# Optimization experiments

Measured on AMD Instinct MI355X. Metric: run time of the kernel, lower is better.

The kernel has to match this reference:

```python
import jax, jax.numpy as jnp
import numpy as np

B, L, H, E, V = 32, 1024, 1024, 512, 8192

def setup_inputs() -> dict:
    key = jax.random.key(0)
    k1, k2, k3, k4 = jax.random.split(key, 4)
    x = jax.random.randint(k1, (B, L), 0, V)
    hidden = jnp.zeros((B, H), dtype=jnp.float32)  # equivalent to hidden=None path
    embedding = jax.random.normal(k2, (V, E), dtype=jnp.float32)
    W_h = jax.random.normal(k3, (E + H, H), dtype=jnp.float32) * 0.01
    b_h = jnp.zeros((H,), dtype=jnp.float32)
    W_o = jax.random.normal(k4, (H, V), dtype=jnp.float32) * 0.01
    b_o = jnp.zeros((V,), dtype=jnp.float32)
    return {"x": x, "hidden": hidden, "embedding": embedding,
            "W_h": W_h, "b_h": b_h, "W_o": W_o, "b_o": b_o}

def reference(x, hidden, embedding, W_h, b_h, W_o, b_o):
    # x: [B, L] int; hidden: [B, H]
    x_embed = embedding[x]                       # [B, L, E]
    x_tl = jnp.swapaxes(x_embed, 0, 1)           # [L, B, E] time-major

    def step(h, x_t):
        # concat + matmul + bias + tanh, one timestep
        combined = jnp.concatenate([x_t, h], axis=1)   # [B, E+H]
        h_new = jnp.tanh(combined @ W_h + b_h)         # [B, H]
        return h_new, h_new

    final_hidden, outs = jax.lax.scan(step, hidden, x_tl)  # outs: [L, B, H]
    output = jnp.swapaxes(outs, 0, 1)                       # [B, L, H]
    logits = output @ W_o + b_o                             # [B, L, V]
    return logits, final_hidden
```

## Files before the change

kernel.cpp:

```cpp
#include <hip/hip_runtime.h>
#include <hip/hip_bf16.h>

typedef unsigned short u16;
typedef unsigned int   u32;
typedef unsigned long long u64;
typedef __attribute__((ext_vector_type(8))) __bf16 bf16x8;
typedef __attribute__((ext_vector_type(4))) float   f32x4;

#define GLOAD16(gp, lp) __builtin_amdgcn_global_load_lds( \
    (__attribute__((address_space(1))) void*)(gp),        \
    (__attribute__((address_space(3))) void*)(lp), 16, 0, 0)

static __device__ __forceinline__ u16 f2bf(float f) {
  __bf16 b = (__bf16)f;
  return __builtin_bit_cast(u16, b);
}
static __device__ __forceinline__ f32x4 mfma16(bf16x8 a, bf16x8 b, f32x4 c) {
  return __builtin_amdgcn_mfma_f32_16x16x32_bf16(a, b, c, 0, 0, 0);
}


__global__ __launch_bounds__(256) void k_cvt_emb(const float* __restrict__ s,
                                                 u16* __restrict__ d) {
  int i = (blockIdx.x * 256 + threadIdx.x) * 4;
  float4 v = *(const float4*)(s + i);
  d[i] = f2bf(v.x); d[i+1] = f2bf(v.y); d[i+2] = f2bf(v.z); d[i+3] = f2bf(v.w);
}

__global__ __launch_bounds__(256) void k_tr_wh(const float* __restrict__ Wh,
                                               u16* __restrict__ WhxT,
                                               u16* __restrict__ WhhT) {
  __shared__ float tile[32][33];
  int bx = blockIdx.x & 31;
  int be = blockIdx.x >> 5;
  int tx = threadIdx.x & 31, ty = threadIdx.x >> 5;
  #pragma unroll
  for (int s = 0; s < 32; s += 8)
    tile[ty + s][tx] = Wh[(size_t)(be*32 + ty + s) * 1024 + bx*32 + tx];
  __syncthreads();
  #pragma unroll
  for (int s = 0; s < 32; s += 8) {
    int e = be*32 + tx;
    int j = bx*32 + ty + s;
    u16 v = f2bf(tile[tx][ty + s]);
    if (e < 512) WhxT[(size_t)j * 512 + e] = v;
    else         WhhT[(size_t)j * 1024 + (e - 512)] = v;
  }
}

__global__ __launch_bounds__(256) void k_tr_wo(const float* __restrict__ Wo,
                                               u16* __restrict__ WoT) {
  __shared__ float tile[32][33];
  int bx = blockIdx.x & 255;
  int by = blockIdx.x >> 8;
  int tx = threadIdx.x & 31, ty = threadIdx.x >> 5;
  #pragma unroll
  for (int s = 0; s < 32; s += 8)
    tile[ty + s][tx] = Wo[(size_t)(by*32 + ty + s) * 8192 + bx*32 + tx];
  __syncthreads();
  #pragma unroll
  for (int s = 0; s < 32; s += 8)
    WoT[(size_t)(bx*32 + ty + s) * 1024 + by*32 + tx] = f2bf(tile[tx][ty + s]);
}

__global__ __launch_bounds__(256) void k_init(const float* __restrict__ hid,
                                              u16* __restrict__ ring,
                                              unsigned* __restrict__ flags) {
  int i = blockIdx.x * 256 + threadIdx.x;
  ring[i] = f2bf(hid[i]);
  if (blockIdx.x < 8) flags[i] = 0;
}

__global__ __launch_bounds__(256) void k_xpart(const int* __restrict__ xq,
                                               const u16* __restrict__ embB,
                                               const u16* __restrict__ WhxT,
                                               const float* __restrict__ bh,
                                               float* __restrict__ xpart) {
  __shared__ __align__(16) u16 As[128 * 32];
  __shared__ __align__(16) u16 Bs[128 * 32];
  __shared__ int sx[128];
  int bid = blockIdx.x;
  int cpx = gridDim.x >> 3;
  int swz = (bid & 7) * cpx + (bid >> 3);
  int tm = (swz >> 3) * 128, tn = (swz & 7) * 128;
  int tid = threadIdx.x, lane = tid & 63, w = tid >> 6;
  int wm = (w >> 1) * 64, wn = (w & 1) * 64;
  if (tid < 128) sx[tid] = xq[tm + tid];
  __syncthreads();
  int r0 = tid >> 2, sub = tid & 3;
  const u16* ga0 = embB + (size_t)sx[r0] * 512 + sub * 8;
  const u16* ga1 = embB + (size_t)sx[64 + r0] * 512 + sub * 8;
  const u16* gb0 = WhxT + (size_t)(tn + r0) * 512 + sub * 8;
  const u16* gb1 = WhxT + (size_t)(tn + 64 + r0) * 512 + sub * 8;
  f32x4 acc[4][4] = {};
  int rl = lane & 15, kb = (lane >> 4) * 8;
  for (int kt = 0; kt < 16; ++kt) {
    int k0 = kt * 32;
    __syncthreads();
    GLOAD16(ga0 + k0, As + w * 512);
    GLOAD16(ga1 + k0, As + 2048 + w * 512);
    GLOAD16(gb0 + k0, Bs + w * 512);
    GLOAD16(gb1 + k0, Bs + 2048 + w * 512);
    __syncthreads();
    bf16x8 af[4], bf[4];
    #pragma unroll
    for (int mi = 0; mi < 4; mi++) af[mi] = *(const bf16x8*)&As[(wm + mi*16 + rl) * 32 + kb];
    #pragma unroll
    for (int ni = 0; ni < 4; ni++) bf[ni] = *(const bf16x8*)&Bs[(wn + ni*16 + rl) * 32 + kb];
    #pragma unroll
    for (int mi = 0; mi < 4; mi++)
      #pragma unroll
      for (int ni = 0; ni < 4; ni++)
        acc[mi][ni] = mfma16(af[mi], bf[ni], acc[mi][ni]);
  }
  int rq = (lane >> 4) << 2;
  #pragma unroll
  for (int ni = 0; ni < 4; ni++) {
    int col = tn + wn + ni*16 + rl;
    float bias = bh[col];
    #pragma unroll
    for (int mi = 0; mi < 4; mi++) {
      int row = tm + wm + mi*16 + rq;
      #pragma unroll
      for (int r = 0; r < 4; r++)
        xpart[(size_t)(row + r) * 1024 + col] = acc[mi][ni][r] + bias;
    }
  }
}

__global__ __launch_bounds__(256) void k_rnn(const u16* __restrict__ WhhT,
                                             const float* __restrict__ xpart,
                                             u16* __restrict__ ring,
                                             float* __restrict__ hfinal,
                                             unsigned* __restrict__ flags) {
  __shared__ __align__(16) float psh[2048];
  int bid = blockIdx.x, tid = threadIdx.x, lane = tid & 63, w = tid >> 6;
  int jbase = bid * 16;
  const int rl = lane & 15;
  const int kbase = w * 256 + ((lane >> 4) << 3);
  bf16x8 Wreg[8];
  #pragma unroll
  for (int ki = 0; ki < 8; ++ki)
    Wreg[ki] = *(const bf16x8*)&WhhT[(size_t)(jbase + rl) * 1024 + kbase + ki * 32];
  const bool red = (tid < 128);
  int b = 0, jq = 0, mi = 0, lsrc = 0, rg = 0;
  float4 xpre = make_float4(0.f, 0.f, 0.f, 0.f);
  if (red) {
    b = tid >> 2; jq = (tid & 3) << 2;
    mi = b >> 4;
    int bb = b & 15;
    lsrc = (bb >> 2) << 4;
    rg = bb & 3;
    xpre = *(const float4*)&xpart[(size_t)(b * 1024 + 0) * 1024 + jbase + jq];
  }
  for (int t = 0; t < 1024; ++t) {
    const u16* hprev = ring + (size_t)t * 32768;
    bf16x8 ha[16];
    #pragma unroll
    for (int ki = 0; ki < 8; ++ki) {
      int k = kbase + ki * 32;
      ha[ki*2 + 0] = *(const bf16x8*)&hprev[(size_t)rl * 1024 + k];
      ha[ki*2 + 1] = *(const bf16x8*)&hprev[(size_t)(16 + rl) * 1024 + k];
    }
    f32x4 acc0 = {0.f, 0.f, 0.f, 0.f}, acc1 = {0.f, 0.f, 0.f, 0.f};
    #pragma unroll
    for (int ki = 0; ki < 8; ++ki) {
      acc0 = mfma16(ha[ki*2 + 0], Wreg[ki], acc0);
      acc1 = mfma16(ha[ki*2 + 1], Wreg[ki], acc1);
    }
    *(f32x4*)&psh[((w * 2 + 0) * 64 + lane) * 4] = acc0;
    *(f32x4*)&psh[((w * 2 + 1) * 64 + lane) * 4] = acc1;
    __syncthreads();
    if (red) {
      float s0 = 0.f, s1 = 0.f, s2 = 0.f, s3 = 0.f;
      #pragma unroll
      for (int ww = 0; ww < 4; ++ww) {
        const float* pp = &psh[((ww * 2 + mi) * 64) * 4];
        s0 += pp[(lsrc + jq + 0) * 4 + rg];
        s1 += pp[(lsrc + jq + 1) * 4 + rg];
        s2 += pp[(lsrc + jq + 2) * 4 + rg];
        s3 += pp[(lsrc + jq + 3) * 4 + rg];
      }
      float v0 = tanhf(s0 + xpre.x);
      float v1 = tanhf(s1 + xpre.y);
      float v2 = tanhf(s2 + xpre.z);
      float v3 = tanhf(s3 + xpre.w);
      u32 lo = (u32)f2bf(v0) | ((u32)f2bf(v1) << 16);
      u32 hi = (u32)f2bf(v2) | ((u32)f2bf(v3) << 16);
      u64 hv = (u64)lo | ((u64)hi << 32);
      __hip_atomic_store((u64*)(ring + (size_t)(t + 1) * 32768 + b * 1024 + jbase + jq),
                         hv, __ATOMIC_RELAXED, __HIP_MEMORY_SCOPE_AGENT);
      if (t == 1023)
        *(float4*)&hfinal[b * 1024 + jbase + jq] = make_float4(v0, v1, v2, v3);
    }
    if (t < 1023) {
      asm volatile("s_waitcnt vmcnt(0)" ::: "memory");
      __syncthreads();
      if (tid == 0)
        __hip_atomic_store(&flags[bid * 32], (unsigned)(t + 1),
                           __ATOMIC_RELAXED, __HIP_MEMORY_SCOPE_AGENT);
      if (red)
        xpre = *(const float4*)&xpart[((size_t)(b * 1024 + (t + 1))) * 1024 + jbase + jq];
      if (w == 0) {
        while (__hip_atomic_load(&flags[lane * 32], __ATOMIC_RELAXED,
                                 __HIP_MEMORY_SCOPE_AGENT) < (unsigned)(t + 1)) { }
      }
      __syncthreads();
    }
  }
}

__global__ __launch_bounds__(256) void k_logits(const u16* __restrict__ A,
                                                const u16* __restrict__ BT,
                                                const float* __restrict__ bo,
                                                float* __restrict__ C) {
  __shared__ __align__(16) u16 As[128 * 32];
  __shared__ __align__(16) u16 Bs[128 * 32];
  int bid = blockIdx.x;
  int cpx = gridDim.x >> 3;
  int swz = (bid & 7) * cpx + (bid >> 3);
  int tm = (swz >> 6) * 128, tn = (swz & 63) * 128;
  int tid = threadIdx.x, lane = tid & 63, w = tid >> 6;
  int wm = (w >> 1) * 64, wn = (w & 1) * 64;
  int r0 = tid >> 2, sub = tid & 3;
  const u16* ga0 = A + (size_t)(tm + r0) * 1024 + sub * 8;
  const u16* ga1 = A + (size_t)(tm + 64 + r0) * 1024 + sub * 8;
  const u16* gb0 = BT + (size_t)(tn + r0) * 1024 + sub * 8;
  const u16* gb1 = BT + (size_t)(tn + 64 + r0) * 1024 + sub * 8;
  f32x4 acc[4][4] = {};
  int rl = lane & 15, kb = (lane >> 4) * 8;
  for (int kt = 0; kt < 32; ++kt) {
    int k0 = kt * 32;
    __syncthreads();
    GLOAD16(ga0 + k0, As + w * 512);
    GLOAD16(ga1 + k0, As + 2048 + w * 512);
    GLOAD16(gb0 + k0, Bs + w * 512);
    GLOAD16(gb1 + k0, Bs + 2048 + w * 512);
    __syncthreads();
    bf16x8 af[4], bf[4];
    #pragma unroll
    for (int mi = 0; mi < 4; mi++) af[mi] = *(const bf16x8*)&As[(wm + mi*16 + rl) * 32 + kb];
    #pragma unroll
    for (int ni = 0; ni < 4; ni++) bf[ni] = *(const bf16x8*)&Bs[(wn + ni*16 + rl) * 32 + kb];
    #pragma unroll
    for (int mi = 0; mi < 4; mi++)
      #pragma unroll
      for (int ni = 0; ni < 4; ni++)
        acc[mi][ni] = mfma16(af[mi], bf[ni], acc[mi][ni]);
  }
  int rq = (lane >> 4) << 2;
  #pragma unroll
  for (int ni = 0; ni < 4; ni++) {
    int col = tn + wn + ni*16 + rl;
    float bias = bo[col];
    #pragma unroll
    for (int mi = 0; mi < 4; mi++) {
      int row = tm + wm + mi*16 + rq;
      #pragma unroll
      for (int r = 0; r < 4; r++) {
        int m = row + r;
        size_t orow = (size_t)(((m & 31) << 10) | (m >> 5));
        C[orow * 8192 + col] = acc[mi][ni][r] + bias;
      }
    }
  }
}

extern "C" void kernel_launch(void* const* d_in, const int* in_sizes, int n_in,
                              void* d_out, int out_size, void* d_ws, size_t ws_size,
                              hipStream_t stream) {
  const int*   x   = (const int*)  d_in[0];
  const float* hid = (const float*)d_in[1];
  const float* emb = (const float*)d_in[2];
  const float* Wh  = (const float*)d_in[3];
  const float* bh  = (const float*)d_in[4];
  const float* Wo  = (const float*)d_in[5];
  const float* bo  = (const float*)d_in[6];
  float* logits = (float*)d_out;
  float* hfinal = logits + (size_t)32768 * 8192;

  char* ws = (char*)d_ws;
  size_t off = 0;
  auto alloc = [&](size_t bytes) {
    char* p = ws + off;
    off += (bytes + 255) & ~(size_t)255;
    return p;
  };
  u16*   embB  = (u16*)  alloc((size_t)8192 * 512 * 2);
  u16*   WhxT  = (u16*)  alloc((size_t)1024 * 512 * 2);
  u16*   WhhT  = (u16*)  alloc((size_t)1024 * 1024 * 2);
  u16*   WoT   = (u16*)  alloc((size_t)8192 * 1024 * 2);
  float* xpart = (float*)alloc((size_t)32768 * 1024 * 4);
  u16*   ring  = (u16*)  alloc((size_t)1025 * 32768 * 2);
  unsigned* flags = (unsigned*)alloc(8192);
  (void)ws_size; (void)in_sizes; (void)n_in; (void)out_size;

  k_cvt_emb<<<4096, 256, 0, stream>>>(emb, embB);
  k_tr_wh  <<<1536, 256, 0, stream>>>(Wh, WhxT, WhhT);
  k_tr_wo  <<<8192, 256, 0, stream>>>(Wo, WoT);
  k_init   <<<128,  256, 0, stream>>>(hid, ring, flags);
  k_xpart  <<<2048, 256, 0, stream>>>(x, embB, WhxT, bh, xpart);
  k_rnn    <<<64,   256, 0, stream>>>(WhhT, xpart, ring, hfinal, flags);
  k_logits <<<16384,256, 0, stream>>>(ring + 32768, WoT, bo, logits);
}
```

Baseline: 5.116 ms.

## Restructure RNN recurrence to 16 blocks with full-K per wave, drop LDS reduction

The persistent recurrent kernel now runs 16 blocks of 512 threads instead of 64 blocks of 256. Each wave owns a 16-column by 16-batch tile and holds that tile's full K range of W_hh in registers (32 bf16x8 fragments). This removes the shared-memory partial-sum reduction and one barrier per timestep. With four times fewer blocks, the inter-block flag barrier polls only 16 flags. In exchange each wave issues more MFMAs and h loads serially per step, register pressure rises, and only 16 CUs do the recurrence.

```diff
diff --git a/kernel.cpp b/kernel.cpp
--- a/kernel.cpp
+++ b/kernel.cpp
@@ -128,82 +128,77 @@
   }
 }
 
-__global__ __launch_bounds__(256) void k_rnn(const u16* __restrict__ WhhT,
-                                             const float* __restrict__ xpart,
-                                             u16* __restrict__ ring,
-                                             float* __restrict__ hfinal,
-                                             unsigned* __restrict__ flags) {
-  __shared__ __align__(16) float psh[2048];
-  int bid = blockIdx.x, tid = threadIdx.x, lane = tid & 63, w = tid >> 6;
-  int jbase = bid * 16;
-  const int rl = lane & 15;
-  const int kbase = w * 256 + ((lane >> 4) << 3);
-  bf16x8 Wreg[8];
-  #pragma unroll
-  for (int ki = 0; ki < 8; ++ki)
-    Wreg[ki] = *(const bf16x8*)&WhhT[(size_t)(jbase + rl) * 1024 + kbase + ki * 32];
-  const bool red = (tid < 128);
-  int b = 0, jq = 0, mi = 0, lsrc = 0, rg = 0;
-  float4 xpre = make_float4(0.f, 0.f, 0.f, 0.f);
-  if (red) {
-    b = tid >> 2; jq = (tid & 3) << 2;
-    mi = b >> 4;
-    int bb = b & 15;
-    lsrc = (bb >> 2) << 4;
-    rg = bb & 3;
-    xpre = *(const float4*)&xpart[(size_t)(b * 1024 + 0) * 1024 + jbase + jq];
-  }
+__global__ __launch_bounds__(512, 2) void k_rnn(const u16* __restrict__ WhhT,
+                                                const float* __restrict__ xpart,
+                                                u16* __restrict__ ring,
+                                                float* __restrict__ hfinal,
+                                                unsigned* __restrict__ flags) {
+  const int bid = blockIdx.x, tid = threadIdx.x;
+  const int lane = tid & 63, wv = tid >> 6;
+  const int jt = wv >> 1, bt = wv & 1;
+  const int rl = lane & 15, kq = lane >> 4;
+  const int kb = kq * 8;
+  const int jbase = bid * 64;
+  const int jA = jbase + jt * 16 + rl;
+  const int bB = bt * 16 + rl;
+  const int j0 = jbase + jt * 16 + kq * 4;
+
+  bf16x8 Wreg[32];
+  { const u16* wp = WhhT + (size_t)jA * 1024 + kb;
+    #pragma unroll
+    for (int kt = 0; kt < 32; ++kt) Wreg[kt] = *(const bf16x8*)(wp + kt * 32); }
+
+  float4 xpre = *(const float4*)&xpart[(size_t)bB * 1048576 + j0];
+
   for (int t = 0; t < 1024; ++t) {
-    const u16* hprev = ring + (size_t)t * 32768;
-    bf16x8 ha[16];
-    #pragma unroll
-    for (int ki = 0; ki < 8; ++ki) {
-      int k = kbase + ki * 32;
-      ha[ki*2 + 0] = *(const bf16x8*)&hprev[(size_t)rl * 1024 + k];
-      ha[ki*2 + 1] = *(const bf16x8*)&hprev[(size_t)(16 + rl) * 1024 + k];
-    }
-    f32x4 acc0 = {0.f, 0.f, 0.f, 0.f}, acc1 = {0.f, 0.f, 0.f, 0.f};
-    #pragma unroll
-    for (int ki = 0; ki < 8; ++ki) {
-      acc0 = mfma16(ha[ki*2 + 0], Wreg[ki], acc0);
-      acc1 = mfma16(ha[ki*2 + 1], Wreg[ki], acc1);
-    }
-    *(f32x4*)&psh[((w * 2 + 0) * 64 + lane) * 4] = acc0;
-    *(f32x4*)&psh[((w * 2 + 1) * 64 + lane) * 4] = acc1;
-    __syncthreads();
-    if (red) {
-      float s0 = 0.f, s1 = 0.f, s2 = 0.f, s3 = 0.f;
-      #pragma unroll
-      for (int ww = 0; ww < 4; ++ww) {
-        const float* pp = &psh[((ww * 2 + mi) * 64) * 4];
-        s0 += pp[(lsrc + jq + 0) * 4 + rg];
-        s1 += pp[(lsrc + jq + 1) * 4 + rg];
-        s2 += pp[(lsrc + jq + 2) * 4 + rg];
-        s3 += pp[(lsrc + jq + 3) * 4 + rg];
+    const u16* hp = ring + (size_t)t * 32768 + (size_t)bB * 1024 + kb;
+    f32x4 a0 = {0.f,0.f,0.f,0.f}, a1 = {0.f,0.f,0.f,0.f};
+    {
+      bf16x8 ha[16];
+      #pragma unroll
+      for (int kt = 0; kt < 16; ++kt) ha[kt] = *(const bf16x8*)(hp + kt * 32);
+      #pragma unroll
+      for (int kt = 0; kt < 16; kt += 2) {
+        a0 = mfma16(Wreg[kt],     ha[kt],     a0);
+        a1 = mfma16(Wreg[kt + 1], ha[kt + 1], a1);
       }
-      float v0 = tanhf(s0 + xpre.x);
-      float v1 = tanhf(s1 + xpre.y);
-      float v2 = tanhf(s2 + xpre.z);
-      float v3 = tanhf(s3 + xpre.w);
-      u32 lo = (u32)f2bf(v0) | ((u32)f2bf(v1) << 16);
-      u32 hi = (u32)f2bf(v2) | ((u32)f2bf(v3) << 16);
-      u64 hv = (u64)lo | ((u64)hi << 32);
-      __hip_atomic_store((u64*)(ring + (size_t)(t + 1) * 32768 + b * 1024 + jbase + jq),
-                         hv, __ATOMIC_RELAXED, __HIP_MEMORY_SCOPE_AGENT);
-      if (t == 1023)
-        *(float4*)&hfinal[b * 1024 + jbase + jq] = make_float4(v0, v1, v2, v3);
-    }
-    if (t < 1023) {
+    }
+    {
+      bf16x8 ha[16];
+      #pragma unroll
+      for (int kt = 0; kt < 16; ++kt) ha[kt] = *(const bf16x8*)(hp + 512 + kt * 32);
+      #pragma unroll
+      for (int kt = 0; kt < 16; kt += 2) {
+        a0 = mfma16(Wreg[16 + kt], ha[kt],     a0);
+        a1 = mfma16(Wreg[17 + kt], ha[kt + 1], a1);
+      }
+    }
+    f32x4 s = a0 + a1;
+    float v0 = tanhf(s[0] + xpre.x);
+    float v1 = tanhf(s[1] + xpre.y);
+    float v2 = tanhf(s[2] + xpre.z);
+    float v3 = tanhf(s[3] + xpre.w);
+    u32 lo = (u32)f2bf(v0) | ((u32)f2bf(v1) << 16);
+    u32 hi = (u32)f2bf(v2) | ((u32)f2bf(v3) << 16);
+    u64 hv = (u64)lo | ((u64)hi << 32);
+    __hip_atomic_store((u64*)(ring + (size_t)(t + 1) * 32768 + (size_t)bB * 1024 + j0),
+                       hv, __ATOMIC_RELAXED, __HIP_MEMORY_SCOPE_AGENT);
+    if (t == 1023) {
+      *(float4*)&hfinal[(size_t)bB * 1024 + j0] = make_float4(v0, v1, v2, v3);
+    } else {
       asm volatile("s_waitcnt vmcnt(0)" ::: "memory");
       __syncthreads();
       if (tid == 0)
         __hip_atomic_store(&flags[bid * 32], (unsigned)(t + 1),
                            __ATOMIC_RELAXED, __HIP_MEMORY_SCOPE_AGENT);
-      if (red)
-        xpre = *(const float4*)&xpart[((size_t)(b * 1024 + (t + 1))) * 1024 + jbase + jq];
-      if (w == 0) {
-        while (__hip_atomic_load(&flags[lane * 32], __ATOMIC_RELAXED,
-                                 __HIP_MEMORY_SCOPE_AGENT) < (unsigned)(t + 1)) { }
+      xpre = *(const float4*)&xpart[(size_t)bB * 1048576 + (size_t)(t + 1) * 1024 + j0];
+      if (wv == 0) {
+        unsigned tgt = (unsigned)(t + 1);
+        for (;;) {
+          unsigned v = __hip_atomic_load(&flags[(lane & 15) * 32], __ATOMIC_RELAXED,
+                                         __HIP_MEMORY_SCOPE_AGENT);
+          if (!__any((int)(v < tgt))) break;
+        }
       }
       __syncthreads();
     }
@@ -300,6 +295,6 @@
   k_tr_wo  <<<8192, 256, 0, stream>>>(Wo, WoT);
   k_init   <<<128,  256, 0, stream>>>(hid, ring, flags);
   k_xpart  <<<2048, 256, 0, stream>>>(x, embB, WhxT, bh, xpart);
-  k_rnn    <<<64,   256, 0, stream>>>(WhhT, xpart, ring, hfinal, flags);
+  k_rnn    <<<16,   512, 0, stream>>>(WhhT, xpart, ring, hfinal, flags);
   k_logits <<<16384,256, 0, stream>>>(ring + 32768, WoT, bo, logits);
 }
```

New measurement: 10.09 ms. 97.2% more time.

## Gate logits tiles on per-timestep RNN progress flags to allow overlap

Applied to the files above, without the earlier changes.

The logits GEMM now waits on per-block RNN progress flags before each tile starts. It only waits until the timesteps covering its 128 rows are published, with the RNN also posting a final flag at the last step. The block-index swizzle is replaced by a time-major tile order so early tiles depend on early timesteps. Both kernels are still launched on the same stream, so real overlap depends on concurrent execution the launch does not request. Otherwise this adds polling and loses the L2-friendly swizzle.

```diff
diff --git a/kernel.cpp b/kernel.cpp
--- a/kernel.cpp
+++ b/kernel.cpp
@@ -17,6 +17,12 @@
 }
 static __device__ __forceinline__ f32x4 mfma16(bf16x8 a, bf16x8 b, f32x4 c) {
   return __builtin_amdgcn_mfma_f32_16x16x32_bf16(a, b, c, 0, 0, 0);
+}
+static __device__ __forceinline__ bf16x8 ald16(const u16* p) {
+  union { u64 q[2]; bf16x8 v; } u;
+  u.q[0] = __hip_atomic_load((const u64*)p,       __ATOMIC_RELAXED, __HIP_MEMORY_SCOPE_AGENT);
+  u.q[1] = __hip_atomic_load((const u64*)(p + 4), __ATOMIC_RELAXED, __HIP_MEMORY_SCOPE_AGENT);
+  return u.v;
 }
 
 
@@ -206,6 +212,12 @@
                                  __HIP_MEMORY_SCOPE_AGENT) < (unsigned)(t + 1)) { }
       }
       __syncthreads();
+    } else {
+      asm volatile("s_waitcnt vmcnt(0)" ::: "memory");
+      __syncthreads();
+      if (tid == 0)
+        __hip_atomic_store(&flags[bid * 32], 1024u,
+                           __ATOMIC_RELAXED, __HIP_MEMORY_SCOPE_AGENT);
     }
   }
 }
@@ -213,14 +225,24 @@
 __global__ __launch_bounds__(256) void k_logits(const u16* __restrict__ A,
                                                 const u16* __restrict__ BT,
                                                 const float* __restrict__ bo,
-                                                float* __restrict__ C) {
+                                                float* __restrict__ C,
+                                                const unsigned* __restrict__ flags) {
   __shared__ __align__(16) u16 As[128 * 32];
   __shared__ __align__(16) u16 Bs[128 * 32];
   int bid = blockIdx.x;
-  int cpx = gridDim.x >> 3;
-  int swz = (bid & 7) * cpx + (bid >> 3);
-  int tm = (swz >> 6) * 128, tn = (swz & 63) * 128;
+  int tIdx = bid >> 6, vIdx = bid & 63;
+  int tm = tIdx * 128, tn = vIdx * 128;
   int tid = threadIdx.x, lane = tid & 63, w = tid >> 6;
+  if (tid < 64) {
+    unsigned tgt = (unsigned)(tIdx * 4 + 4);
+    const unsigned* fp = flags + tid * 32;
+    for (;;) {
+      unsigned v = __hip_atomic_load(fp, __ATOMIC_RELAXED, __HIP_MEMORY_SCOPE_AGENT);
+      if (!__any((int)(v < tgt))) break;
+      __builtin_amdgcn_s_sleep(32);
+    }
+  }
+  __syncthreads();
   int wm = (w >> 1) * 64, wn = (w & 1) * 64;
   int r0 = tid >> 2, sub = tid & 3;
   const u16* ga0 = A + (size_t)(tm + r0) * 1024 + sub * 8;
@@ -301,5 +323,5 @@
   k_init   <<<128,  256, 0, stream>>>(hid, ring, flags);
   k_xpart  <<<2048, 256, 0, stream>>>(x, embB, WhxT, bh, xpart);
   k_rnn    <<<64,   256, 0, stream>>>(WhhT, xpart, ring, hfinal, flags);
-  k_logits <<<16384,256, 0, stream>>>(ring + 32768, WoT, bo, logits);
-}
+  k_logits <<<16384,256, 0, stream>>>(ring + 32768, WoT, bo, logits, flags);
+}
```

Measured after the change: 5.004 ms. 2.2% less time.
